# Kernel optimization log

Measured on AMD Instinct MI355X. Metric: run time of the kernel, lower is better.

Reference implementation:

```python
import jax, jax.numpy as jnp
import numpy as np

MARGIN = 0.1
EPS = 1e-6
NUM_COMPARE = 5
N, D = 32768, 512


def setup_inputs() -> dict:
    key = jax.random.key(0)
    k1, k2 = jax.random.split(key)
    output = jax.random.normal(k1, (N, D), dtype=jnp.float32)
    target = jax.random.normal(k2, (N, D), dtype=jnp.float32)
    return {"output": output, "target": target}


def reference(output, target):
    # torch CosineSimilarity(dim=0, eps=1e-6): dot(x,y) / max(||x||*||y||, eps)
    n = output.shape[0]
    on = jnp.linalg.norm(output, axis=-1)          # [N]
    tn = jnp.linalg.norm(target, axis=-1)          # [N]
    # positive similarity: cos(target[i], output[i])
    pos = jnp.sum(output * target, axis=-1) / jnp.maximum(on * tn, EPS)  # [N]
    # negative similarities: cos(target[j], output[i]) for j in 0..NUM_COMPARE-1
    t5 = target[:NUM_COMPARE]                      # [5, D]
    tn5 = tn[:NUM_COMPARE]                         # [5]
    S = (output @ t5.T) / jnp.maximum(on[:, None] * tn5[None, :], EPS)   # [N, 5]
    # mask out j == i (only affects first NUM_COMPARE rows)
    i_idx = jnp.arange(n)[:, None]
    j_idx = jnp.arange(NUM_COMPARE)[None, :]
    mask = (i_idx != j_idx).astype(output.dtype)   # [N, 5]
    hinge = jax.nn.relu(MARGIN - pos[:, None] + S) * mask
    count = n * NUM_COMPARE - min(n, NUM_COMPARE)  # pairs with j != i
    return jnp.sum(hinge) / count
```

## Files before the change

kernel.cpp:

```cpp
#include <hip/hip_runtime.h>


constexpr int D   = 512;
constexpr int NC  = 5;
constexpr float MARGIN_F = 0.1f;
constexpr float EPS_F    = 1e-6f;

__device__ __forceinline__ float dot4(const float4 a, const float4 b) {
  return a.x*b.x + a.y*b.y + a.z*b.z + a.w*b.w;
}

template <int CTRL>
__device__ __forceinline__ float dpp_add(float x) {
  const int y = __builtin_amdgcn_update_dpp(
      0, __float_as_int(x), CTRL, 0xF, 0xF, true);
  return x + __int_as_float(y);
}

__device__ __forceinline__ float red64(float x) {
  x = dpp_add<0xB1>(x);
  x = dpp_add<0x4E>(x);
  x = dpp_add<0x124>(x);
  x = dpp_add<0x128>(x);
  x += __shfl_xor(x, 16);
  x += __shfl_xor(x, 32);
  return x;
}

__global__ __launch_bounds__(320) void tn5_kernel(
    const float* __restrict__ tgt, float* __restrict__ tn5_out)
{
  const int w = threadIdx.x >> 6, lane = threadIdx.x & 63;
  const float4* tp = reinterpret_cast<const float4*>(tgt) + w * 128;
  const float4 a = tp[lane], b = tp[64 + lane];
  const float s = red64(dot4(a, a) + dot4(b, b));
  if (lane == 0) tn5_out[w] = sqrtf(s);
}

__global__ __launch_bounds__(256) void hinge_kernel(
    const float* __restrict__ out, const float* __restrict__ tgt,
    const float* __restrict__ tn5g, float* __restrict__ partial, int n)
{
  const int tid  = threadIdx.x;
  const int wid  = tid >> 6;
  const int lane = tid & 63;
  const int row  = blockIdx.x * 4 + wid;
  __shared__ float bsum[4];

  float h = 0.f;
  if (row < n) {
    const float4* op = reinterpret_cast<const float4*>(out) + (size_t)row * 128;
    const float4* tp = reinterpret_cast<const float4*>(tgt) + (size_t)row * 128;
    const float4 o0 = op[lane], o1 = op[64 + lane];
    const float4 t0 = tp[lane], t1 = tp[64 + lane];

    const float4* t5p = reinterpret_cast<const float4*>(tgt);
    float s_ot = dot4(o0, t0) + dot4(o1, t1);
    float s_oo = dot4(o0, o0) + dot4(o1, o1);
    float s_tt = dot4(t0, t0) + dot4(t1, t1);
    float s5[NC];
    #pragma unroll
    for (int j = 0; j < NC; ++j) {
      const float4 v0 = t5p[j * 128 + lane];
      const float4 v1 = t5p[j * 128 + 64 + lane];
      s5[j] = dot4(o0, v0) + dot4(o1, v1);
    }

    s_ot = red64(s_ot);
    s_oo = red64(s_oo);
    s_tt = red64(s_tt);
    #pragma unroll
    for (int j = 0; j < NC; ++j) s5[j] = red64(s5[j]);

    if (lane == 0) {
      const float on  = sqrtf(s_oo);
      const float tn  = sqrtf(s_tt);
      const float pos = s_ot / fmaxf(on * tn, EPS_F);
      #pragma unroll
      for (int j = 0; j < NC; ++j) {
        const float S = s5[j] / fmaxf(on * tn5g[j], EPS_F);
        const float hv = fmaxf(0.f, MARGIN_F - pos + S);
        h += (row == j) ? 0.f : hv;
      }
    }
  }
  if (lane == 0) bsum[wid] = h;
  __syncthreads();
  if (tid == 0) partial[blockIdx.x] = bsum[0] + bsum[1] + bsum[2] + bsum[3];
}

__global__ __launch_bounds__(256) void reduce_kernel(
    const float* __restrict__ part, float* __restrict__ result,
    int nw, float inv_count)
{
  float s = 0.f;
  for (int i = threadIdx.x; i < nw; i += 256) s += part[i];
  s = red64(s);
  __shared__ float ws[4];
  if ((threadIdx.x & 63) == 0) ws[threadIdx.x >> 6] = s;
  __syncthreads();
  if (threadIdx.x == 0) result[0] = (ws[0] + ws[1] + ws[2] + ws[3]) * inv_count;
}

extern "C" void kernel_launch(void* const* d_in, const int* in_sizes, int n_in,
                              void* d_out, int out_size, void* d_ws, size_t ws_size,
                              hipStream_t stream) {
  const float* out = (const float*)d_in[0];
  const float* tgt = (const float*)d_in[1];
  float* result   = (float*)d_out;
  float* partials = (float*)d_ws;
  float* tn5_ws   = partials + 8192;

  const int n = in_sizes[0] / D;
  const int blocks = (n + 3) / 4;
  const long long count = (long long)n * NC - (n < NC ? n : NC);
  const float inv_count = 1.0f / (float)count;

  tn5_kernel<<<1, 320, 0, stream>>>(tgt, tn5_ws);
  hinge_kernel<<<blocks, 256, 0, stream>>>(out, tgt, tn5_ws, partials, n);
  reduce_kernel<<<1, 256, 0, stream>>>(partials, result, blocks, inv_count);
}
```

Measured before the change: 148.6 us.

## Process four rows per wave with register prefetch and hoisted target-5 loads

The hinge kernel now runs a fixed grid of 2048 blocks, and each wave loops over four consecutive rows. The next row's output and target vectors are loaded while the current row is being reduced. The five comparison target rows and their norms are loaded into registers once per wave instead of once per row, which cuts redundant L2 traffic. The aim is to keep more memory requests in flight and hide load latency. The cost is higher register pressure, and the four-iteration loop with a fixed grid only covers n up to 32768 rows.

```diff
diff --git a/kernel.cpp b/kernel.cpp
--- a/kernel.cpp
+++ b/kernel.cpp
@@ -44,27 +44,49 @@
   const int tid  = threadIdx.x;
   const int wid  = tid >> 6;
   const int lane = tid & 63;
-  const int row  = blockIdx.x * 4 + wid;
-  __shared__ float bsum[4];
+  const int gwave = blockIdx.x * 4 + wid;
+  const int nw    = gridDim.x * 4;
+  const int rpw   = (n + nw - 1) / nw;
 
-  float h = 0.f;
-  if (row < n) {
-    const float4* op = reinterpret_cast<const float4*>(out) + (size_t)row * 128;
-    const float4* tp = reinterpret_cast<const float4*>(tgt) + (size_t)row * 128;
-    const float4 o0 = op[lane], o1 = op[64 + lane];
-    const float4 t0 = tp[lane], t1 = tp[64 + lane];
+  const float4* op  = reinterpret_cast<const float4*>(out);
+  const float4* tp  = reinterpret_cast<const float4*>(tgt);
 
-    const float4* t5p = reinterpret_cast<const float4*>(tgt);
-    float s_ot = dot4(o0, t0) + dot4(o1, t1);
-    float s_oo = dot4(o0, o0) + dot4(o1, o1);
-    float s_tt = dot4(t0, t0) + dot4(t1, t1);
+  float4 t5r[NC][2];
+  #pragma unroll
+  for (int j = 0; j < NC; ++j) {
+    t5r[j][0] = tp[j * 128 + lane];
+    t5r[j][1] = tp[j * 128 + 64 + lane];
+  }
+  float tn5[NC];
+  #pragma unroll
+  for (int j = 0; j < NC; ++j) tn5[j] = tn5g[j];
+
+  const int row0 = gwave * rpw;
+
+  float4 co0, co1, ct0, ct1;
+  {
+    const size_t r = (size_t)min(row0, n - 1) * 128;
+    co0 = op[r + lane];  co1 = op[r + 64 + lane];
+    ct0 = tp[r + lane];  ct1 = tp[r + 64 + lane];
+  }
+
+  float acc = 0.f;
+  #pragma unroll
+  for (int it = 0; it < 4; ++it) {
+    float4 no0, no1, nt0, nt1;
+    if (it < 3) {
+      const size_t r = (size_t)min(row0 + it + 1, n - 1) * 128;
+      no0 = op[r + lane];  no1 = op[r + 64 + lane];
+      nt0 = tp[r + lane];  nt1 = tp[r + 64 + lane];
+    }
+
+    float s_ot = dot4(co0, ct0) + dot4(co1, ct1);
+    float s_oo = dot4(co0, co0) + dot4(co1, co1);
+    float s_tt = dot4(ct0, ct0) + dot4(ct1, ct1);
     float s5[NC];
     #pragma unroll
-    for (int j = 0; j < NC; ++j) {
-      const float4 v0 = t5p[j * 128 + lane];
-      const float4 v1 = t5p[j * 128 + 64 + lane];
-      s5[j] = dot4(o0, v0) + dot4(o1, v1);
-    }
+    for (int j = 0; j < NC; ++j)
+      s5[j] = dot4(co0, t5r[j][0]) + dot4(co1, t5r[j][1]);
 
     s_ot = red64(s_ot);
     s_oo = red64(s_oo);
@@ -72,19 +94,23 @@
     #pragma unroll
     for (int j = 0; j < NC; ++j) s5[j] = red64(s5[j]);
 
-    if (lane == 0) {
+    const int row = row0 + it;
+    if (row < n) {
       const float on  = sqrtf(s_oo);
       const float tn  = sqrtf(s_tt);
       const float pos = s_ot / fmaxf(on * tn, EPS_F);
       #pragma unroll
       for (int j = 0; j < NC; ++j) {
-        const float S = s5[j] / fmaxf(on * tn5g[j], EPS_F);
+        const float S = s5[j] / fmaxf(on * tn5[j], EPS_F);
         const float hv = fmaxf(0.f, MARGIN_F - pos + S);
-        h += (row == j) ? 0.f : hv;
+        acc += (row == j) ? 0.f : hv;
       }
     }
+    co0 = no0; co1 = no1; ct0 = nt0; ct1 = nt1;
   }
-  if (lane == 0) bsum[wid] = h;
+
+  __shared__ float bsum[4];
+  if (lane == 0) bsum[wid] = acc;
   __syncthreads();
   if (tid == 0) partial[blockIdx.x] = bsum[0] + bsum[1] + bsum[2] + bsum[3];
 }
@@ -109,10 +135,10 @@
   const float* tgt = (const float*)d_in[1];
   float* result   = (float*)d_out;
   float* partials = (float*)d_ws;
-  float* tn5_ws   = partials + 8192;
+  float* tn5_ws   = partials + 2048;
 
   const int n = in_sizes[0] / D;
-  const int blocks = (n + 3) / 4;
+  const int blocks = 2048;
   const long long count = (long long)n * NC - (n < NC ? n : NC);
   const float inv_count = 1.0f / (float)count;
 
```

Result: no change. 151.5 us (+2.0%).
